# Performance work log

Hardware: AMD Instinct MI355X
Metric: run time of the kernel (lower is better)

Reference implementation:

```python
import jax, jax.numpy as jnp
import numpy as np

B, S, D = 2, 2048, 1024
H = 16
HD = D // H
MLP = 4096
EPS = 1e-5


def _layernorm(x, g, b):
    mu = jnp.mean(x, axis=-1, keepdims=True)
    var = jnp.mean(jnp.square(x - mu), axis=-1, keepdims=True)
    return (x - mu) * jax.lax.rsqrt(var + EPS) * g + b


def setup_inputs() -> dict:
    key = jax.random.key(0)
    ks = jax.random.split(key, 16)
    sd = 0.02
    return {
        "x": jax.random.normal(ks[0], (B, S, D), jnp.float32),
        "dis_attn_mask": jax.random.normal(ks[1], (B, S, S), jnp.float32) * 0.1,
        "cls_attn_mask": jax.random.normal(ks[2], (B, S, S), jnp.float32) * 0.1,
        "wq": jax.random.normal(ks[3], (D, D), jnp.float32) * sd,
        "bq": jnp.zeros((D,), jnp.float32),
        "wk": jax.random.normal(ks[4], (D, D), jnp.float32) * sd,
        "bk": jnp.zeros((D,), jnp.float32),
        "wv": jax.random.normal(ks[5], (D, D), jnp.float32) * sd,
        "bv": jnp.zeros((D,), jnp.float32),
        "ln1_g": jnp.ones((D,), jnp.float32),
        "ln1_b": jnp.zeros((D,), jnp.float32),
        "ln2_g": jnp.ones((D,), jnp.float32),
        "ln2_b": jnp.zeros((D,), jnp.float32),
        "w1": jax.random.normal(ks[6], (D, MLP), jnp.float32) * sd,
        "b1": jnp.zeros((MLP,), jnp.float32),
        "w2": jax.random.normal(ks[7], (MLP, D), jnp.float32) * sd,
        "b2": jnp.zeros((D,), jnp.float32),
    }


def reference(x, dis_attn_mask, cls_attn_mask, wq, bq, wk, bk, wv, bv,
              ln1_g, ln1_b, ln2_g, ln2_b, w1, b1, w2, b2):
    res = x
    h = _layernorm(x, ln1_g, ln1_b)
    q = h @ wq + bq
    k = h @ wk + bk
    v = h @ wv + bv
    # NOTE: original torch code uses .view(B, H, S, HD) on a contiguous
    # [B, S, D] tensor (no transpose); row-major reshape reproduces this.
    q = q.reshape(B, H, S, HD)
    k = k.reshape(B, H, S, HD)
    v = v.reshape(B, H, S, HD)
    w = jnp.einsum('bhsd,bhtd->bhst', q, k) * (HD ** -0.5)
    w = w + dis_attn_mask[:, None] + cls_attn_mask[:, None]
    w = jax.nn.softmax(w, axis=-1)
    h_attn = jnp.einsum('bhst,bhtd->bhsd', w, v).reshape(B, S, D)
    h = h_attn + res
    h = _layernorm(h, ln2_g, ln2_b)
    res2 = h
    h = jax.nn.gelu(h @ w1 + b1, approximate=False) @ w2 + b2
    return h + res2
```

## Files before the change

kernel.cpp:

```cpp
#include <hip/hip_runtime.h>
#include <hip/hip_bf16.h>
#include <math.h>

#define BB 2
#define SS 2048
#define DD 1024
#define HH 16
#define MLPD 4096

typedef __attribute__((ext_vector_type(8))) short bf16x8;
typedef __attribute__((ext_vector_type(4))) float f32x4;
typedef __attribute__((ext_vector_type(4))) unsigned short us4;

static __device__ __forceinline__ float fast_exp2(float x) {
#if __has_builtin(__builtin_amdgcn_exp2f)
  return __builtin_amdgcn_exp2f(x);
#else
  return exp2f(x);
#endif
}
static __device__ __forceinline__ float fast_rcp(float x) {
#if __has_builtin(__builtin_amdgcn_rcpf)
  return __builtin_amdgcn_rcpf(x);
#else
  return 1.0f / x;
#endif
}

static __device__ __forceinline__ unsigned short f2bf(float f) {
  union { float f; unsigned int u; } v; v.f = f;
  unsigned int r = v.u + 0x7fffu + ((v.u >> 16) & 1u);
  return (unsigned short)(r >> 16);
}
static __device__ __forceinline__ float bf2f(unsigned short b) {
  return __uint_as_float(((unsigned int)b) << 16);
}

static __device__ __forceinline__ float gelu_f(float x) {
  float u = x * x;
  float z = x * fmaf(u, 0.0713548162f, 1.59576912f);
  float e = fast_exp2(z * -1.44269504f);
  return x * fast_rcp(1.0f + e);
}

static __device__ __forceinline__ int swz(int row) {
  return (row & 3) ^ ((row >> 2) & 3);
}

static __device__ __forceinline__ void async16(const unsigned short* g, unsigned short* l) {
  __builtin_amdgcn_global_load_lds(
      (const __attribute__((address_space(1))) unsigned int*)g,
      (__attribute__((address_space(3))) unsigned int*)l, 16, 0, 0);
}

__global__ __launch_bounds__(256) void transpose_to_bf16(
    const float* __restrict__ src, unsigned short* __restrict__ dst,
    int K, int N) {
  __shared__ float tile[32][33];
  int t = threadIdx.x;
  int c = t & 31, rl = t >> 5;
  int bx = blockIdx.x, by = blockIdx.y;
#pragma unroll
  for (int i = 0; i < 4; ++i) {
    int row = rl * 4 + i;
    tile[row][c] = src[(size_t)(by * 32 + row) * N + bx * 32 + c];
  }
  __syncthreads();
#pragma unroll
  for (int i = 0; i < 4; ++i) {
    int n = rl * 4 + i;
    dst[(size_t)(bx * 32 + n) * K + by * 32 + c] = f2bf(tile[c][n]);
  }
}

__global__ __launch_bounds__(256) void transpose_qkv(
    const float* __restrict__ wq, const float* __restrict__ wk,
    const float* __restrict__ wv, unsigned short* __restrict__ dst) {
  __shared__ float tile[32][33];
  const float* src = blockIdx.z == 0 ? wq : blockIdx.z == 1 ? wk : wv;
  unsigned short* d = dst + (size_t)blockIdx.z * 1024 * 1024;
  int t = threadIdx.x;
  int c = t & 31, rl = t >> 5;
  int bx = blockIdx.x, by = blockIdx.y;
#pragma unroll
  for (int i = 0; i < 4; ++i) {
    int row = rl * 4 + i;
    tile[row][c] = src[(size_t)(by * 32 + row) * DD + bx * 32 + c];
  }
  __syncthreads();
#pragma unroll
  for (int i = 0; i < 4; ++i) {
    int n = rl * 4 + i;
    d[(size_t)(bx * 32 + n) * DD + by * 32 + c] = f2bf(tile[c][n]);
  }
}

__global__ __launch_bounds__(256) void concat_bias(
    const float* __restrict__ bq, const float* __restrict__ bk,
    const float* __restrict__ bv, float* __restrict__ dst) {
  int i = blockIdx.x * 256 + threadIdx.x;
  if (i < 1024) dst[i] = bq[i];
  else if (i < 2048) dst[i] = bk[i - 1024];
  else if (i < 3072) dst[i] = bv[i - 2048];
}

__global__ __launch_bounds__(256) void mask_prep3(
    const float* __restrict__ dis, const float* __restrict__ cls,
    unsigned short* __restrict__ cmP) {
  __shared__ unsigned short sm[16][512];
  int qtO = blockIdx.x, waveO = blockIdx.y;
  int b = blockIdx.z >> 2, ktg = blockIdx.z & 3;
  int t = threadIdx.x;
  int row0 = qtO * 128 + waveO * 16;
  int col0 = ktg * 512;
  const float* db = dis + (size_t)b * SS * SS;
  const float* cb = cls + (size_t)b * SS * SS;
  int lrow = t >> 4, lcg = t & 15;
#pragma unroll
  for (int shot = 0; shot < 8; ++shot) {
    int cc = lcg * 4 + shot * 64;
    size_t idx = (size_t)(row0 + lrow) * SS + col0 + cc;
    float4 d4 = *(const float4*)(db + idx);
    float4 c4 = *(const float4*)(cb + idx);
    us4 o;
    o[0] = f2bf((d4.x + c4.x) * 8.0f);
    o[1] = f2bf((d4.y + c4.y) * 8.0f);
    o[2] = f2bf((d4.z + c4.z) * 8.0f);
    o[3] = f2bf((d4.w + c4.w) * 8.0f);
    *(us4*)&sm[lrow][cc] = o;
  }
  __syncthreads();
  int ktL = t >> 5, lp = t & 31;
  unsigned short* ob =
      cmP + ((((size_t)b * 16 + qtO) * 8 + waveO) * 32 + ktg * 8 + ktL) * 64 * 16;
#pragma unroll
  for (int li = 0; li < 2; ++li) {
    int l = lp * 2 + li;
    int g = l >> 4, c16 = l & 15;
    short v[16];
#pragma unroll
    for (int t4 = 0; t4 < 4; ++t4)
#pragma unroll
      for (int r = 0; r < 4; ++r)
        v[t4 * 4 + r] = (short)sm[g * 4 + r][ktL * 64 + t4 * 16 + c16];
    unsigned short* o = ob + (size_t)l * 16;
    *(bf16x8*)(o) = *(bf16x8*)&v[0];
    *(bf16x8*)(o + 8) = *(bf16x8*)&v[8];
  }
}

template <bool BF_IN, bool ADD>
__global__ __launch_bounds__(256) void ln_bf16(
    const void* __restrict__ in, const float* __restrict__ add,
    const float* __restrict__ g, const float* __restrict__ beta,
    unsigned short* __restrict__ out) {
  int row = blockIdx.x;
  int t = threadIdx.x;
  float x[4];
  if (BF_IN) {
    us4 b4 = *(const us4*)((const unsigned short*)in + (size_t)row * DD + t * 4);
#pragma unroll
    for (int i = 0; i < 4; ++i) x[i] = bf2f(b4[i]);
  } else {
    float4 f4 = *(const float4*)((const float*)in + (size_t)row * DD + t * 4);
    x[0] = f4.x; x[1] = f4.y; x[2] = f4.z; x[3] = f4.w;
  }
  if (ADD) {
    float4 a4 = *(const float4*)(add + (size_t)row * DD + t * 4);
    x[0] += a4.x; x[1] += a4.y; x[2] += a4.z; x[3] += a4.w;
  }
  float s1 = x[0] + x[1] + x[2] + x[3];
  float s2 = x[0] * x[0] + x[1] * x[1] + x[2] * x[2] + x[3] * x[3];
#pragma unroll
  for (int off = 32; off > 0; off >>= 1) {
    s1 += __shfl_down(s1, off);
    s2 += __shfl_down(s2, off);
  }
  __shared__ float sa[4], sb[4];
  int wid = t >> 6;
  if ((t & 63) == 0) { sa[wid] = s1; sb[wid] = s2; }
  __syncthreads();
  s1 = sa[0] + sa[1] + sa[2] + sa[3];
  s2 = sb[0] + sb[1] + sb[2] + sb[3];
  float mean = s1 * (1.0f / 1024.0f);
  float var = s2 * (1.0f / 1024.0f) - mean * mean;
  float rstd = rsqrtf(var + 1e-5f);
  float4 gv = *(const float4*)(g + t * 4);
  float4 bv = *(const float4*)(beta + t * 4);
  us4 o;
  o[0] = f2bf((x[0] - mean) * rstd * gv.x + bv.x);
  o[1] = f2bf((x[1] - mean) * rstd * gv.y + bv.y);
  o[2] = f2bf((x[2] - mean) * rstd * gv.z + bv.z);
  o[3] = f2bf((x[3] - mean) * rstd * gv.w + bv.w);
  *(us4*)(out + (size_t)row * DD + t * 4) = o;
}

template <int BN, bool GELU, bool ADDSRC, bool OUT_BF16, bool SPLIT3>
__global__ __launch_bounds__(256) void gemm_bf16(
    const unsigned short* __restrict__ A, const unsigned short* __restrict__ BT,
    const float* __restrict__ bias, const unsigned short* __restrict__ addsrc,
    void* C0, void* C1, void* C2, int M, int N, int K) {
  constexpr int BJ = BN / 32;
  constexpr int BCH = BN / 64;
  __shared__ __align__(16) unsigned short As[128][32];
  __shared__ __align__(16) unsigned short Bs[BN][32];
  int tid = threadIdx.x;
  int wave = tid >> 6, lane = tid & 63;
  int g = lane >> 4, c16 = lane & 15;
  int nwg = gridDim.x * gridDim.y;
  int wg = blockIdx.y * gridDim.x + blockIdx.x;
  int cpx = nwg >> 3;
  int sw = (wg & 7) * cpx + (wg >> 3);
  int bxs = sw % gridDim.x, bys = sw / gridDim.x;
  int m0 = bys * 128, n0 = bxs * BN;
  int wm = (wave >> 1) * 64, wn = (wave & 1) * (BN / 2);
  int lrow = lane >> 2, lq = lane & 3;
  int dq = (lq ^ swz(lrow)) * 8;
  const unsigned short* aS = A + (size_t)(m0 + wave * 32 + lrow) * K + lq * 8;
  unsigned short* aD0 = &As[wave * 32 + lrow][dq];
  unsigned short* aD1 = &As[wave * 32 + 16 + lrow][dq];
  const unsigned short* bS = BT + (size_t)(n0 + wave * (BCH * 16) + lrow) * K + lq * 8;
  unsigned short* bD0 = &Bs[wave * (BCH * 16) + lrow][dq];
  unsigned short* bD1 = &Bs[(wave * (BCH * 16) + 16 + lrow) % BN][dq];
  int vA = (g ^ swz(c16)) * 8;
  const int KI = K / 32;
  const size_t rK = 16 * (size_t)K;

  bf16x8 a0a = *(const bf16x8*)(aS);
  bf16x8 a1a = *(const bf16x8*)(aS + rK);
  bf16x8 b0a = *(const bf16x8*)(bS);
  bf16x8 b1a;
  if constexpr (BCH == 2) b1a = *(const bf16x8*)(bS + rK);
  bf16x8 a0b = *(const bf16x8*)(aS + 32);
  bf16x8 a1b = *(const bf16x8*)(aS + rK + 32);
  bf16x8 b0b = *(const bf16x8*)(bS + 32);
  bf16x8 b1b;
  if constexpr (BCH == 2) b1b = *(const bf16x8*)(bS + rK + 32);

  f32x4 acc[4][BJ] = {};
  for (int kt = 0; kt < KI; kt += 2) {
    __syncthreads();
    *(bf16x8*)aD0 = a0a;
    *(bf16x8*)aD1 = a1a;
    *(bf16x8*)bD0 = b0a;
    if constexpr (BCH == 2) *(bf16x8*)bD1 = b1a;
    __syncthreads();
    if (kt + 2 < KI) {
      int ko = (kt + 2) * 32;
      a0a = *(const bf16x8*)(aS + ko);
      a1a = *(const bf16x8*)(aS + rK + ko);
      b0a = *(const bf16x8*)(bS + ko);
      if constexpr (BCH == 2) b1a = *(const bf16x8*)(bS + rK + ko);
    }
    {
      bf16x8 a[4], b[BJ];
#pragma unroll
      for (int i = 0; i < 4; ++i) a[i] = *(const bf16x8*)&As[wm + i * 16 + c16][vA];
#pragma unroll
      for (int j = 0; j < BJ; ++j) b[j] = *(const bf16x8*)&Bs[wn + j * 16 + c16][vA];
#pragma unroll
      for (int i = 0; i < 4; ++i)
#pragma unroll
        for (int j = 0; j < BJ; ++j)
          acc[i][j] = __builtin_amdgcn_mfma_f32_16x16x32_bf16(a[i], b[j], acc[i][j], 0, 0, 0);
    }
    __syncthreads();
    *(bf16x8*)aD0 = a0b;
    *(bf16x8*)aD1 = a1b;
    *(bf16x8*)bD0 = b0b;
    if constexpr (BCH == 2) *(bf16x8*)bD1 = b1b;
    __syncthreads();
    if (kt + 3 < KI) {
      int ko = (kt + 3) * 32;
      a0b = *(const bf16x8*)(aS + ko);
      a1b = *(const bf16x8*)(aS + rK + ko);
      b0b = *(const bf16x8*)(bS + ko);
      if constexpr (BCH == 2) b1b = *(const bf16x8*)(bS + rK + ko);
    }
    {
      bf16x8 a[4], b[BJ];
#pragma unroll
      for (int i = 0; i < 4; ++i) a[i] = *(const bf16x8*)&As[wm + i * 16 + c16][vA];
#pragma unroll
      for (int j = 0; j < BJ; ++j) b[j] = *(const bf16x8*)&Bs[wn + j * 16 + c16][vA];
#pragma unroll
      for (int i = 0; i < 4; ++i)
#pragma unroll
        for (int j = 0; j < BJ; ++j)
          acc[i][j] = __builtin_amdgcn_mfma_f32_16x16x32_bf16(a[i], b[j], acc[i][j], 0, 0, 0);
    }
  }
  unsigned short* dstb = nullptr;
  int lc0 = 0;
  if (SPLIT3) {
    int which = n0 >> 10;
    dstb = (unsigned short*)(which == 0 ? C0 : which == 1 ? C1 : C2);
    lc0 = n0 & 1023;
  }
#pragma unroll
  for (int j = 0; j < BJ; ++j) {
    int coff = wn + j * 16 + c16;
    float bj = bias[n0 + coff];
#pragma unroll
    for (int i = 0; i < 4; ++i) {
#pragma unroll
      for (int r = 0; r < 4; ++r) {
        int row = m0 + wm + i * 16 + g * 4 + r;
        float cval = acc[i][j][r] + bj;
        if (GELU) cval = gelu_f(cval);
        if (ADDSRC) cval += bf2f(addsrc[(size_t)row * N + n0 + coff]);
        if (SPLIT3) {
          dstb[(size_t)row * 1024 + lc0 + coff] = f2bf(cval);
        } else if (OUT_BF16) {
          ((unsigned short*)C0)[(size_t)row * N + n0 + coff] = f2bf(cval);
        } else {
          ((float*)C0)[(size_t)row * N + n0 + coff] = cval;
        }
      }
    }
  }
}

#define VMW(n) asm volatile("s_waitcnt vmcnt(" #n ")" ::: "memory")
#define BARX() do { asm volatile("" ::: "memory"); \
                    __builtin_amdgcn_s_barrier(); \
                    asm volatile("" ::: "memory"); } while (0)

template <bool GELU, bool SPLIT3>
__global__ __launch_bounds__(512, 2) void gemm256(
    const unsigned short* __restrict__ A, const unsigned short* __restrict__ BT,
    const float* __restrict__ bias, void* C0, void* C1, void* C2,
    int N, int K) {
  __shared__ __align__(16) char lds[2][2][2][16384];
  int tid = threadIdx.x;
  int lane = tid & 63, w = tid >> 6;
  int g = lane >> 4, c16 = lane & 15;
  int wm16 = (w >> 2) << 4;
  int wn16 = (w & 3) << 4;
  int nwg = gridDim.x * gridDim.y;
  int wg = blockIdx.y * gridDim.x + blockIdx.x;
  int cpx = nwg >> 3;
  int sw = (wg & 7) * cpx + (wg >> 3);
  int bx = sw % gridDim.x, by = sw / gridDim.x;
  int m0 = by << 8, n0 = bx << 8;

  int st0 = tid >> 6, ci0 = tid & 63;
  int cp0 = ci0 ^ (((ci0 >> 5) & 1) << 1);
  int sr0 = ((st0 >> 1) << 4) + (cp0 >> 2);
  int sk0 = ((st0 & 1) << 5) + ((cp0 & 3) << 3);
  size_t soff = (size_t)sr0 * K + sk0;

  auto stage = [&](int op, int h, int tt, int d) {
    const unsigned short* base = (op == 0 ? A : BT);
    int row0 = (op == 0 ? m0 : n0) + (h << 7);
    const unsigned short* src = base + (size_t)row0 * K + (tt << 6) + soff;
    unsigned short* dst = (unsigned short*)&lds[op][d][h][tid * 16];
    async16(src, dst);
    async16(src + ((size_t)K << 6), dst + 4096);
  };

  auto foff = [&](int r, int ke) -> int {
    int stt = ((r >> 4) << 1) + (ke >> 5);
    int loc = ((r & 15) << 6) + ((ke & 31) << 1);
    return (stt << 10) + (loc ^ (((r >> 3) & 1) << 5));
  };
  int offA[4][2], offB[2][2];
#pragma unroll
  for (int ii = 0; ii < 4; ++ii)
#pragma unroll
    for (int ks = 0; ks < 2; ++ks)
      offA[ii][ks] = foff(ii * 32 + wm16 + c16, ks * 32 + g * 8);
#pragma unroll
  for (int jj = 0; jj < 2; ++jj)
#pragma unroll
    for (int ks = 0; ks < 2; ++ks)
      offB[jj][ks] = foff(jj * 64 + wn16 + c16, ks * 32 + g * 8);

  f32x4 acc[8][4] = {};

#define MFMA_Q(IH, JH, AF, BF) do {                                           \
    __builtin_amdgcn_s_setprio(1);                                            \
    _Pragma("unroll") for (int ii = 0; ii < 4; ++ii)                          \
      _Pragma("unroll") for (int jj = 0; jj < 2; ++jj) {                      \
        acc[(IH)*4+ii][(JH)*2+jj] = __builtin_amdgcn_mfma_f32_16x16x32_bf16(  \
            AF[ii][0], BF[jj][0], acc[(IH)*4+ii][(JH)*2+jj], 0, 0, 0);        \
        acc[(IH)*4+ii][(JH)*2+jj] = __builtin_amdgcn_mfma_f32_16x16x32_bf16(  \
            AF[ii][1], BF[jj][1], acc[(IH)*4+ii][(JH)*2+jj], 0, 0, 0);        \
      }                                                                       \
    __builtin_amdgcn_s_setprio(0);                                            \
  } while (0)

  stage(0, 0, 0, 0);
  stage(1, 0, 0, 0);
  stage(0, 1, 0, 0);
  stage(1, 1, 0, 0);
  VMW(4);
  BARX();

  const int KT = K >> 6;
  for (int kt = 0; kt < KT; ++kt) {
    int d = kt & 1, dn = d ^ 1;
    int t1 = kt + 1 < KT ? kt + 1 : KT - 1;
    const char* pd = &lds[0][d][0][0];
    bf16x8 A0f[4][2], A1f[4][2], Bf[2][2];

#pragma unroll
    for (int ii = 0; ii < 4; ++ii)
#pragma unroll
      for (int ks = 0; ks < 2; ++ks)
        A0f[ii][ks] = *(const bf16x8*)(pd + offA[ii][ks]);
#pragma unroll
    for (int jj = 0; jj < 2; ++jj)
#pragma unroll
      for (int ks = 0; ks < 2; ++ks)
        Bf[jj][ks] = *(const bf16x8*)(pd + 65536 + offB[jj][ks]);
    stage(0, 0, t1, dn);
    stage(1, 0, t1, dn);
    VMW(6);
    BARX();
    MFMA_Q(0, 0, A0f, Bf);
    BARX();

#pragma unroll
    for (int ii = 0; ii < 4; ++ii)
#pragma unroll
      for (int ks = 0; ks < 2; ++ks)
        A1f[ii][ks] = *(const bf16x8*)(pd + 16384 + offA[ii][ks]);
    stage(0, 1, t1, dn);
    VMW(6);
    BARX();
    MFMA_Q(1, 0, A1f, Bf);
    BARX();

#pragma unroll
    for (int jj = 0; jj < 2; ++jj)
#pragma unroll
      for (int ks = 0; ks < 2; ++ks)
        Bf[jj][ks] = *(const bf16x8*)(pd + 81920 + offB[jj][ks]);
    stage(1, 1, t1, dn);
    BARX();
    MFMA_Q(1, 1, A1f, Bf);
    BARX();

    VMW(4);
    BARX();
    MFMA_Q(0, 1, A0f, Bf);
    BARX();
  }
#undef MFMA_Q
  VMW(0);

  unsigned short* dstb = nullptr;
  int lc0 = 0;
  if (SPLIT3) {
    int which = n0 >> 10;
    dstb = (unsigned short*)(which == 0 ? C0 : which == 1 ? C1 : C2);
    lc0 = n0 & 1023;
  }
#pragma unroll
  for (int i = 0; i < 8; ++i) {
#pragma unroll
    for (int j = 0; j < 4; ++j) {
      int row_b = m0 + ((i >> 2) << 7) + ((i & 3) << 5) + wm16 + (g << 2);
      int colp = ((j >> 1) << 7) + ((j & 1) << 6) + wn16 + c16;
      float bj = bias[n0 + colp];
#pragma unroll
      for (int r = 0; r < 4; ++r) {
        float cv = acc[i][j][r] + bj;
        if (GELU) cv = gelu_f(cv);
        int row = row_b + r;
        if (SPLIT3) {
          dstb[(size_t)row * 1024 + lc0 + colp] = f2bf(cv);
        } else {
          ((unsigned short*)C0)[(size_t)row * N + n0 + colp] = f2bf(cv);
        }
      }
    }
  }
}

__global__ __launch_bounds__(512) void attn_mfma(
    const unsigned short* __restrict__ q, const unsigned short* __restrict__ k,
    const unsigned short* __restrict__ v, const unsigned short* __restrict__ cmP,
    unsigned short* __restrict__ outO) {
  __shared__ __align__(16) unsigned short Ks[2][64][32];
  __shared__ __align__(16) unsigned short Vt[64][72];
  __shared__ __align__(16) unsigned short Ps[128][72];
  int tid = threadIdx.x;
  int wave = tid >> 6, lane = tid & 63;
  int g = lane >> 4, c16 = lane & 15;
  int qt = blockIdx.x, h = blockIdx.y, b = blockIdx.z;
  int s0 = qt * 128;
  int wr = wave * 16;
  size_t headoff = (size_t)b * SS * DD + (size_t)h * SS * 64;
  const unsigned short* qb = q + headoff;
  const unsigned short* kb = k + headoff;
  const unsigned short* vb = v + headoff;
  const unsigned short* csrc =
      cmP + ((((size_t)b * 16 + qt) * 8 + wave) * 32 * 64 + lane) * 16;

  int kkey = tid >> 3, kseg = tid & 7;
  unsigned short* kdst = &Ks[kseg >> 2][kkey][((kseg & 3) ^ swz(kkey)) * 8];
  const unsigned short* ksrc = kb + (size_t)kkey * 64 + kseg * 8;
  const unsigned short* vsrc = vb + (size_t)lane * 64 + wave * 8;
  int vK = (g ^ swz(c16)) * 8;

  bf16x8 qf0, qf1;
  {
    size_t qrow = (size_t)(s0 + wr + c16) * 64;
    qf0 = *(const bf16x8*)(qb + qrow + g * 8);
    qf1 = *(const bf16x8*)(qb + qrow + 32 + g * 8);
  }
  bf16x8 ones;
#pragma unroll
  for (int j = 0; j < 8; ++j) ones[j] = (short)0x3F80;
  f32x4 o[4] = {};
  f32x4 ol = {};
  const float scale2 = 0.18033688f;

  bf16x8 kreg = *(const bf16x8*)(ksrc);
  bf16x8 vreg = *(const bf16x8*)(vsrc);
  bf16x8 cmA = *(const bf16x8*)(csrc);
  bf16x8 cmB = *(const bf16x8*)(csrc + 8);

  for (int kt = 0; kt < 32; ++kt) {
    __syncthreads();
    *(bf16x8*)kdst = kreg;
#pragma unroll
    for (int j = 0; j < 8; ++j) Vt[wave * 8 + j][lane] = (unsigned short)vreg[j];
    __syncthreads();

    int ktn = kt + 1 < 32 ? kt + 1 : 31;
    bf16x8 kregN = *(const bf16x8*)(ksrc + (size_t)ktn * 4096);
    bf16x8 vregN = *(const bf16x8*)(vsrc + (size_t)ktn * 4096);
    bf16x8 cmAN = *(const bf16x8*)(csrc + (size_t)ktn * 1024);
    bf16x8 cmBN = *(const bf16x8*)(csrc + (size_t)ktn * 1024 + 8);

    f32x4 s[4];
#pragma unroll
    for (int r = 0; r < 4; ++r) {
      s[0][r] = bf2f((unsigned short)cmA[r]);
      s[1][r] = bf2f((unsigned short)cmA[4 + r]);
      s[2][r] = bf2f((unsigned short)cmB[r]);
      s[3][r] = bf2f((unsigned short)cmB[4 + r]);
    }
#pragma unroll
    for (int t = 0; t < 4; ++t) {
      bf16x8 b0 = *(const bf16x8*)&Ks[0][t * 16 + c16][vK];
      bf16x8 b1 = *(const bf16x8*)&Ks[1][t * 16 + c16][vK];
      s[t] = __builtin_amdgcn_mfma_f32_16x16x32_bf16(qf0, b0, s[t], 0, 0, 0);
      s[t] = __builtin_amdgcn_mfma_f32_16x16x32_bf16(qf1, b1, s[t], 0, 0, 0);
    }
#pragma unroll
    for (int t = 0; t < 4; ++t)
#pragma unroll
      for (int r = 0; r < 4; ++r) {
        float p = fast_exp2(s[t][r] * scale2);
        Ps[wr + g * 4 + r][t * 16 + c16] = (unsigned short)(__float_as_uint(p) >> 16);
      }
#pragma unroll
    for (int ks = 0; ks < 2; ++ks) {
      bf16x8 pa = *(const bf16x8*)&Ps[wr + c16][ks * 32 + g * 8];
#pragma unroll
      for (int t2 = 0; t2 < 4; ++t2) {
        bf16x8 vb8 = *(const bf16x8*)&Vt[t2 * 16 + c16][ks * 32 + g * 8];
        o[t2] = __builtin_amdgcn_mfma_f32_16x16x32_bf16(pa, vb8, o[t2], 0, 0, 0);
      }
      ol = __builtin_amdgcn_mfma_f32_16x16x32_bf16(pa, ones, ol, 0, 0, 0);
    }
    kreg = kregN;
    vreg = vregN;
    cmA = cmAN;
    cmB = cmBN;
  }
  float inv[4];
#pragma unroll
  for (int r = 0; r < 4; ++r) inv[r] = fast_rcp(ol[r]);
#pragma unroll
  for (int t2 = 0; t2 < 4; ++t2)
#pragma unroll
    for (int r = 0; r < 4; ++r) {
      int srow = s0 + wr + g * 4 + r;
      outO[headoff + (size_t)srow * 64 + t2 * 16 + c16] = f2bf(o[t2][r] * inv[r]);
    }
}

extern "C" void kernel_launch(void* const* d_in, const int* in_sizes, int n_in,
                              void* d_out, int out_size, void* d_ws, size_t ws_size,
                              hipStream_t stream) {
  const float* x    = (const float*)d_in[0];
  const float* dis  = (const float*)d_in[1];
  const float* cls  = (const float*)d_in[2];
  const float* wq   = (const float*)d_in[3];
  const float* bq   = (const float*)d_in[4];
  const float* wk   = (const float*)d_in[5];
  const float* bk   = (const float*)d_in[6];
  const float* wv   = (const float*)d_in[7];
  const float* bv   = (const float*)d_in[8];
  const float* ln1g = (const float*)d_in[9];
  const float* ln1b = (const float*)d_in[10];
  const float* ln2g = (const float*)d_in[11];
  const float* ln2b = (const float*)d_in[12];
  const float* w1   = (const float*)d_in[13];
  const float* b1   = (const float*)d_in[14];
  const float* w2   = (const float*)d_in[15];
  const float* b2   = (const float*)d_in[16];
  float* out = (float*)d_out;
  char* ws = (char*)d_ws;

  unsigned short* qkvwT = (unsigned short*)(ws + 0);
  unsigned short* w1T   = (unsigned short*)(ws + 6291456);
  unsigned short* w2T   = (unsigned short*)(ws + 14680064);
  float*          qkvb  = (float*)(ws + 23068672);
  unsigned short* r1    = (unsigned short*)(ws + 23134208);
  unsigned short* qbuf  = (unsigned short*)(ws + 31522816);
  unsigned short* kbuf  = (unsigned short*)(ws + 39911424);
  unsigned short* vbuf  = (unsigned short*)(ws + 48300032);
  unsigned short* h2    = (unsigned short*)(ws + 56688640);
  unsigned short* cmP   = (unsigned short*)(ws + 65077248);
  unsigned short* mm    = (unsigned short*)(ws + 23134208);
  unsigned short* h1 = r1;
  unsigned short* attnO = r1;

  const int rows = BB * SS;

  transpose_qkv<<<dim3(DD / 32, DD / 32, 3), 256, 0, stream>>>(wq, wk, wv, qkvwT);
  transpose_to_bf16<<<dim3(MLPD / 32, DD / 32), 256, 0, stream>>>(w1, w1T, DD, MLPD);
  transpose_to_bf16<<<dim3(DD / 32, MLPD / 32), 256, 0, stream>>>(w2, w2T, MLPD, DD);
  concat_bias<<<12, 256, 0, stream>>>(bq, bk, bv, qkvb);
  mask_prep3<<<dim3(16, 8, 8), 256, 0, stream>>>(dis, cls, cmP);

  ln_bf16<false, false><<<rows, 256, 0, stream>>>(x, nullptr, ln1g, ln1b, h1);

  gemm256<false, true><<<dim3(3072 / 256, rows / 256), 512, 0, stream>>>(
      h1, qkvwT, qkvb, qbuf, kbuf, vbuf, 3072, DD);

  attn_mfma<<<dim3(SS / 128, HH, BB), 512, 0, stream>>>(qbuf, kbuf, vbuf, cmP, attnO);

  ln_bf16<true, true><<<rows, 256, 0, stream>>>(attnO, x, ln2g, ln2b, h2);

  gemm256<true, false><<<dim3(MLPD / 256, rows / 256), 512, 0, stream>>>(
      h2, w1T, b1, mm, nullptr, nullptr, MLPD, DD);

  gemm_bf16<64, false, true, false, false><<<dim3(DD / 64, rows / 128), 256, 0, stream>>>(
      mm, w2T, b2, h2, out, nullptr, nullptr, rows, DD, MLPD);
}
```

Measured before the change: 389.8 us.

## Double attention query tile per block to 256 rows and remap block order

The attention kernel now handles 256 query rows per block, with each wave computing two 16-row sub-tiles that share the K/V tiles staged in LDS. This halves the K/V global loads and the LDS staging work per query row. Block indices are remapped so that consecutive blocks walk head and batch before the query tile, which is meant to improve mask and KV cache locality. A diagonal column swizzle on the P scratch buffer is meant to reduce LDS bank conflicts. The cost is more registers per wave and half as many blocks (256), which may leave the CUs less busy.

```diff
diff --git a/kernel.cpp b/kernel.cpp
--- a/kernel.cpp
+++ b/kernel.cpp
@@ -479,25 +479,31 @@
   }
 }
 
-__global__ __launch_bounds__(512) void attn_mfma(
+__global__ __launch_bounds__(512) void attn_mfma256(
     const unsigned short* __restrict__ q, const unsigned short* __restrict__ k,
     const unsigned short* __restrict__ v, const unsigned short* __restrict__ cmP,
     unsigned short* __restrict__ outO) {
   __shared__ __align__(16) unsigned short Ks[2][64][32];
   __shared__ __align__(16) unsigned short Vt[64][72];
-  __shared__ __align__(16) unsigned short Ps[128][72];
+  __shared__ __align__(16) unsigned short Ps[256][72];
   int tid = threadIdx.x;
   int wave = tid >> 6, lane = tid & 63;
   int g = lane >> 4, c16 = lane & 15;
-  int qt = blockIdx.x, h = blockIdx.y, b = blockIdx.z;
-  int s0 = qt * 128;
-  int wr = wave * 16;
+  int w = blockIdx.x + 8 * blockIdx.y + 128 * blockIdx.z;
+  int qt = (w >> 4) & 7;
+  int b = (w >> 3) & 1;
+  int h = (w & 7) | (((w >> 7) & 1) << 3);
+  int s0 = qt * 256;
+  int wr = wave * 32;
   size_t headoff = (size_t)b * SS * DD + (size_t)h * SS * 64;
   const unsigned short* qb = q + headoff;
   const unsigned short* kb = k + headoff;
   const unsigned short* vb = v + headoff;
-  const unsigned short* csrc =
-      cmP + ((((size_t)b * 16 + qt) * 8 + wave) * 32 * 64 + lane) * 16;
+  int qtA = qt * 2 + (wave >> 2);
+  int wOA = (wave & 3) * 2;
+  const unsigned short* csrcA =
+      cmP + ((((size_t)b * 16 + qtA) * 8 + wOA) * 2048 + lane) * 16;
+  const unsigned short* csrcB = csrcA + 2048 * 16;
 
   int kkey = tid >> 3, kseg = tid & 7;
   unsigned short* kdst = &Ks[kseg >> 2][kkey][((kseg & 3) ^ swz(kkey)) * 8];
@@ -505,23 +511,28 @@
   const unsigned short* vsrc = vb + (size_t)lane * 64 + wave * 8;
   int vK = (g ^ swz(c16)) * 8;
 
-  bf16x8 qf0, qf1;
+  bf16x8 qf0A, qf1A, qf0B, qf1B;
   {
-    size_t qrow = (size_t)(s0 + wr + c16) * 64;
-    qf0 = *(const bf16x8*)(qb + qrow + g * 8);
-    qf1 = *(const bf16x8*)(qb + qrow + 32 + g * 8);
+    size_t qrowA = (size_t)(s0 + wr + c16) * 64;
+    size_t qrowB = (size_t)(s0 + wr + 16 + c16) * 64;
+    qf0A = *(const bf16x8*)(qb + qrowA + g * 8);
+    qf1A = *(const bf16x8*)(qb + qrowA + 32 + g * 8);
+    qf0B = *(const bf16x8*)(qb + qrowB + g * 8);
+    qf1B = *(const bf16x8*)(qb + qrowB + 32 + g * 8);
   }
   bf16x8 ones;
 #pragma unroll
   for (int j = 0; j < 8; ++j) ones[j] = (short)0x3F80;
-  f32x4 o[4] = {};
-  f32x4 ol = {};
+  f32x4 oA[4] = {}, oB[4] = {};
+  f32x4 olA = {}, olB = {};
   const float scale2 = 0.18033688f;
 
   bf16x8 kreg = *(const bf16x8*)(ksrc);
   bf16x8 vreg = *(const bf16x8*)(vsrc);
-  bf16x8 cmA = *(const bf16x8*)(csrc);
-  bf16x8 cmB = *(const bf16x8*)(csrc + 8);
+  bf16x8 cmA0 = *(const bf16x8*)(csrcA);
+  bf16x8 cmA1 = *(const bf16x8*)(csrcA + 8);
+  bf16x8 cmB0 = *(const bf16x8*)(csrcB);
+  bf16x8 cmB1 = *(const bf16x8*)(csrcB + 8);
 
   for (int kt = 0; kt < 32; ++kt) {
     __syncthreads();
@@ -533,55 +544,77 @@
     int ktn = kt + 1 < 32 ? kt + 1 : 31;
     bf16x8 kregN = *(const bf16x8*)(ksrc + (size_t)ktn * 4096);
     bf16x8 vregN = *(const bf16x8*)(vsrc + (size_t)ktn * 4096);
-    bf16x8 cmAN = *(const bf16x8*)(csrc + (size_t)ktn * 1024);
-    bf16x8 cmBN = *(const bf16x8*)(csrc + (size_t)ktn * 1024 + 8);
-
-    f32x4 s[4];
+    bf16x8 cmA0N = *(const bf16x8*)(csrcA + (size_t)ktn * 1024);
+    bf16x8 cmA1N = *(const bf16x8*)(csrcA + (size_t)ktn * 1024 + 8);
+    bf16x8 cmB0N = *(const bf16x8*)(csrcB + (size_t)ktn * 1024);
+    bf16x8 cmB1N = *(const bf16x8*)(csrcB + (size_t)ktn * 1024 + 8);
+
+    f32x4 sA[4], sB[4];
 #pragma unroll
     for (int r = 0; r < 4; ++r) {
-      s[0][r] = bf2f((unsigned short)cmA[r]);
-      s[1][r] = bf2f((unsigned short)cmA[4 + r]);
-      s[2][r] = bf2f((unsigned short)cmB[r]);
-      s[3][r] = bf2f((unsigned short)cmB[4 + r]);
+      sA[0][r] = bf2f((unsigned short)cmA0[r]);
+      sA[1][r] = bf2f((unsigned short)cmA0[4 + r]);
+      sA[2][r] = bf2f((unsigned short)cmA1[r]);
+      sA[3][r] = bf2f((unsigned short)cmA1[4 + r]);
+      sB[0][r] = bf2f((unsigned short)cmB0[r]);
+      sB[1][r] = bf2f((unsigned short)cmB0[4 + r]);
+      sB[2][r] = bf2f((unsigned short)cmB1[r]);
+      sB[3][r] = bf2f((unsigned short)cmB1[4 + r]);
     }
 #pragma unroll
     for (int t = 0; t < 4; ++t) {
       bf16x8 b0 = *(const bf16x8*)&Ks[0][t * 16 + c16][vK];
       bf16x8 b1 = *(const bf16x8*)&Ks[1][t * 16 + c16][vK];
-      s[t] = __builtin_amdgcn_mfma_f32_16x16x32_bf16(qf0, b0, s[t], 0, 0, 0);
-      s[t] = __builtin_amdgcn_mfma_f32_16x16x32_bf16(qf1, b1, s[t], 0, 0, 0);
-    }
-#pragma unroll
-    for (int t = 0; t < 4; ++t)
+      sA[t] = __builtin_amdgcn_mfma_f32_16x16x32_bf16(qf0A, b0, sA[t], 0, 0, 0);
+      sA[t] = __builtin_amdgcn_mfma_f32_16x16x32_bf16(qf1A, b1, sA[t], 0, 0, 0);
+      sB[t] = __builtin_amdgcn_mfma_f32_16x16x32_bf16(qf0B, b0, sB[t], 0, 0, 0);
+      sB[t] = __builtin_amdgcn_mfma_f32_16x16x32_bf16(qf1B, b1, sB[t], 0, 0, 0);
+    }
+#pragma unroll
+    for (int t = 0; t < 4; ++t) {
+      int colw = ((t + g) & 3) * 16 + c16;
 #pragma unroll
       for (int r = 0; r < 4; ++r) {
-        float p = fast_exp2(s[t][r] * scale2);
-        Ps[wr + g * 4 + r][t * 16 + c16] = (unsigned short)(__float_as_uint(p) >> 16);
+        float pA = fast_exp2(sA[t][r] * scale2);
+        Ps[wr + g * 4 + r][colw] = (unsigned short)(__float_as_uint(pA) >> 16);
+        float pB = fast_exp2(sB[t][r] * scale2);
+        Ps[wr + 16 + g * 4 + r][colw] = (unsigned short)(__float_as_uint(pB) >> 16);
       }
+    }
 #pragma unroll
     for (int ks = 0; ks < 2; ++ks) {
-      bf16x8 pa = *(const bf16x8*)&Ps[wr + c16][ks * 32 + g * 8];
+      int ttc = ((ks * 2 + (g >> 1)) + ((c16 >> 2) & 3)) & 3;
+      int colp = ttc * 16 + (g & 1) * 8;
+      bf16x8 paA = *(const bf16x8*)&Ps[wr + c16][colp];
+      bf16x8 paB = *(const bf16x8*)&Ps[wr + 16 + c16][colp];
 #pragma unroll
       for (int t2 = 0; t2 < 4; ++t2) {
         bf16x8 vb8 = *(const bf16x8*)&Vt[t2 * 16 + c16][ks * 32 + g * 8];
-        o[t2] = __builtin_amdgcn_mfma_f32_16x16x32_bf16(pa, vb8, o[t2], 0, 0, 0);
+        oA[t2] = __builtin_amdgcn_mfma_f32_16x16x32_bf16(paA, vb8, oA[t2], 0, 0, 0);
+        oB[t2] = __builtin_amdgcn_mfma_f32_16x16x32_bf16(paB, vb8, oB[t2], 0, 0, 0);
       }
-      ol = __builtin_amdgcn_mfma_f32_16x16x32_bf16(pa, ones, ol, 0, 0, 0);
+      olA = __builtin_amdgcn_mfma_f32_16x16x32_bf16(paA, ones, olA, 0, 0, 0);
+      olB = __builtin_amdgcn_mfma_f32_16x16x32_bf16(paB, ones, olB, 0, 0, 0);
     }
     kreg = kregN;
     vreg = vregN;
-    cmA = cmAN;
-    cmB = cmBN;
-  }
-  float inv[4];
-#pragma unroll
-  for (int r = 0; r < 4; ++r) inv[r] = fast_rcp(ol[r]);
+    cmA0 = cmA0N; cmA1 = cmA1N;
+    cmB0 = cmB0N; cmB1 = cmB1N;
+  }
+  float invA[4], invB[4];
+#pragma unroll
+  for (int r = 0; r < 4; ++r) {
+    invA[r] = fast_rcp(olA[r]);
+    invB[r] = fast_rcp(olB[r]);
+  }
 #pragma unroll
   for (int t2 = 0; t2 < 4; ++t2)
 #pragma unroll
     for (int r = 0; r < 4; ++r) {
-      int srow = s0 + wr + g * 4 + r;
-      outO[headoff + (size_t)srow * 64 + t2 * 16 + c16] = f2bf(o[t2][r] * inv[r]);
+      int srowA = s0 + wr + g * 4 + r;
+      int srowB = srowA + 16;
+      outO[headoff + (size_t)srowA * 64 + t2 * 16 + c16] = f2bf(oA[t2][r] * invA[r]);
+      outO[headoff + (size_t)srowB * 64 + t2 * 16 + c16] = f2bf(oB[t2][r] * invB[r]);
     }
 }
 
@@ -635,7 +668,8 @@
   gemm256<false, true><<<dim3(3072 / 256, rows / 256), 512, 0, stream>>>(
       h1, qkvwT, qkvb, qbuf, kbuf, vbuf, 3072, DD);
 
-  attn_mfma<<<dim3(SS / 128, HH, BB), 512, 0, stream>>>(qbuf, kbuf, vbuf, cmP, attnO);
+  attn_mfma256<<<dim3(SS / 256, HH, BB), 512, 0, stream>>>(
+      qbuf, kbuf, vbuf, cmP, attnO);
 
   ln_bf16<true, true><<<rows, 256, 0, stream>>>(attnO, x, ln2g, ln2b, h2);
 
```

After: 388.4 us. About the same (-0.3%).
